# Performance work log

Hardware: AMD Instinct MI355X
Metric: run time of the kernel (lower is better)

## Reference

```python
import jax, jax.numpy as jnp
import numpy as np

# HardSimMask config (baked constants, matching init_kwargs and repo semantics)
K = 0.5                 # minimum-percentage-of-space parameter
D = 256                 # embedding dim
MIN_SIM_BOUND = -np.sqrt(D)   # l2 + relu activation -> (min, max) = (-sqrt(d), 0)
MAX_SIM_BOUND = 0.0
MIN_SIM = (MAX_SIM_BOUND - MIN_SIM_BOUND) * K + MIN_SIM_BOUND  # threshold


def setup_inputs() -> dict:
    key = jax.random.key(0)
    k1, k2 = jax.random.split(key)
    x = jax.random.normal(k1, (8192, D), dtype=jnp.float32)
    x_n = jax.random.normal(k2, (8192, D), dtype=jnp.float32)
    return {"x": x, "x_n": x_n}


def _neg_l2_cdist(x, x_n):
    # -||x_i - x_n_j||_2 via the Gram-matrix identity (matches torch.cdist p=2)
    x2 = jnp.sum(x * x, axis=1, keepdims=True)          # [N, 1]
    y2 = jnp.sum(x_n * x_n, axis=1, keepdims=True).T    # [1, M]
    d2 = x2 + y2 - 2.0 * (x @ x_n.T)                    # [N, M]
    return -jnp.sqrt(jnp.maximum(d2, 0.0))


def reference(x, x_n):
    sim = _neg_l2_cdist(x, x_n)                         # [N, M]
    mask = sim < MIN_SIM
    # agg is None: sim - masked_fill(inf) == -inf where masked, sim elsewhere
    return jnp.where(mask, -jnp.inf, sim)
```

## Files before the change

kernel.cpp:

```cpp
#include <hip/hip_runtime.h>
#include <cstdint>

typedef unsigned short u16;
typedef __attribute__((ext_vector_type(8))) __bf16 bf16x8;
typedef __attribute__((ext_vector_type(4))) float f32x4;

#define NROWS 8192
#define KDIM  256
#define BM 128
#define BN 128
#define BK 64

__device__ __forceinline__ u16 f2bf(float f) {
  uint32_t u = __builtin_bit_cast(uint32_t, f);
  return (u16)((u + 0x7fffu + ((u >> 16) & 1u)) >> 16);
}

__global__ void __launch_bounds__(256) prep_kernel(const float* __restrict__ src,
                                                   u16* __restrict__ dst,
                                                   float* __restrict__ norms) {
  const int row  = blockIdx.x * 4 + (threadIdx.x >> 6);
  const int lane = threadIdx.x & 63;
  const float4 v = *reinterpret_cast<const float4*>(&src[row * KDIM + lane * 4]);
  float s = v.x * v.x + v.y * v.y + v.z * v.z + v.w * v.w;
#pragma unroll
  for (int off = 32; off > 0; off >>= 1) s += __shfl_down(s, off, 64);
  ushort4 b;
  b.x = f2bf(v.x); b.y = f2bf(v.y); b.z = f2bf(v.z); b.w = f2bf(v.w);
  *reinterpret_cast<ushort4*>(&dst[row * KDIM + lane * 4]) = b;
  if (lane == 0) norms[row] = s;
}

__global__ void __launch_bounds__(256) gemm_mask_kernel(const u16* __restrict__ A,
                                                        const u16* __restrict__ B,
                                                        const float* __restrict__ x2,
                                                        const float* __restrict__ y2,
                                                        float* __restrict__ out) {
  __shared__ __align__(16) u16 sA[BM * BK];
  __shared__ __align__(16) u16 sB[BN * BK];
  const int tid  = threadIdx.x;
  const int wave = tid >> 6;
  const int lane = tid & 63;
  const int bx = blockIdx.x & 63;
  const int by = blockIdx.x >> 6;
  const int rowBase = by * BM;
  const int colBase = bx * BN;
  const int wr = wave >> 1;
  const int wc = wave & 1;

  f32x4 acc[4][4] = {};

  for (int k0 = 0; k0 < KDIM; k0 += BK) {
#pragma unroll
    for (int it = 0; it < 4; ++it) {
      const int e = it * 2048 + tid * 8;
      const int r = e >> 6;
      const int c = e & 63;
      const int ldsOff = it * 2048 + wave * 512;
      __builtin_amdgcn_global_load_lds(
          (const __attribute__((address_space(1))) void*)&A[(size_t)(rowBase + r) * KDIM + k0 + c],
          (__attribute__((address_space(3))) void*)&sA[ldsOff], 16, 0, 0);
      __builtin_amdgcn_global_load_lds(
          (const __attribute__((address_space(1))) void*)&B[(size_t)(colBase + r) * KDIM + k0 + c],
          (__attribute__((address_space(3))) void*)&sB[ldsOff], 16, 0, 0);
    }
    __syncthreads();

#pragma unroll
    for (int kk = 0; kk < BK; kk += 32) {
      const int kO = kk + (lane >> 4) * 8;
      bf16x8 af[4], bfr[4];
#pragma unroll
      for (int m = 0; m < 4; ++m)
        af[m] = *reinterpret_cast<const bf16x8*>(&sA[(wr * 64 + m * 16 + (lane & 15)) * BK + kO]);
#pragma unroll
      for (int n = 0; n < 4; ++n)
        bfr[n] = *reinterpret_cast<const bf16x8*>(&sB[(wc * 64 + n * 16 + (lane & 15)) * BK + kO]);
#pragma unroll
      for (int m = 0; m < 4; ++m)
#pragma unroll
        for (int n = 0; n < 4; ++n)
          acc[m][n] = __builtin_amdgcn_mfma_f32_16x16x32_bf16(bfr[n], af[m], acc[m][n], 0, 0, 0);
    }
    __syncthreads();
  }

  const float SENTINEL = -3.0e38f;
  float4 yv[4];
#pragma unroll
  for (int n = 0; n < 4; ++n)
    yv[n] = *reinterpret_cast<const float4*>(&y2[colBase + wc * 64 + n * 16 + (lane >> 4) * 4]);
#pragma unroll
  for (int m = 0; m < 4; ++m) {
    const int row = rowBase + wr * 64 + m * 16 + (lane & 15);
    const float xr = x2[row];
    float* orow = out + (size_t)row * NROWS + colBase + wc * 64 + (lane >> 4) * 4;
#pragma unroll
    for (int n = 0; n < 4; ++n) {
      float4 o;
      {
        float d2 = fmaxf(xr + yv[n].x - 2.0f * acc[m][n][0], 0.0f);
        float s  = -__builtin_sqrtf(d2);
        o.x = (s < -8.0f) ? SENTINEL : s;
      }
      {
        float d2 = fmaxf(xr + yv[n].y - 2.0f * acc[m][n][1], 0.0f);
        float s  = -__builtin_sqrtf(d2);
        o.y = (s < -8.0f) ? SENTINEL : s;
      }
      {
        float d2 = fmaxf(xr + yv[n].z - 2.0f * acc[m][n][2], 0.0f);
        float s  = -__builtin_sqrtf(d2);
        o.z = (s < -8.0f) ? SENTINEL : s;
      }
      {
        float d2 = fmaxf(xr + yv[n].w - 2.0f * acc[m][n][3], 0.0f);
        float s  = -__builtin_sqrtf(d2);
        o.w = (s < -8.0f) ? SENTINEL : s;
      }
      *reinterpret_cast<float4*>(&orow[n * 16]) = o;
    }
  }
}

extern "C" void kernel_launch(void* const* d_in, const int* in_sizes, int n_in,
                              void* d_out, int out_size, void* d_ws, size_t ws_size,
                              hipStream_t stream) {
  const float* x  = (const float*)d_in[0];
  const float* xn = (const float*)d_in[1];
  float* out = (float*)d_out;

  u16* Xb = (u16*)d_ws;
  u16* Yb = Xb + (size_t)NROWS * KDIM;
  float* x2 = (float*)(Yb + (size_t)NROWS * KDIM);
  float* y2 = x2 + NROWS;

  prep_kernel<<<NROWS / 4, 256, 0, stream>>>(x, Xb, x2);
  prep_kernel<<<NROWS / 4, 256, 0, stream>>>(xn, Yb, y2);
  gemm_mask_kernel<<<dim3(64 * 64), dim3(256), 0, stream>>>(Xb, Yb, x2, y2, out);
}
```

Before: 89.68 us.

## Make GEMM blocks persistent over column tiles with register-resident A and full-K B staging

Each block now holds its 128-row A panel in registers for the full K=256 and loops over 8 column tiles, staging a whole 128x256 B tile into LDS with an XOR swizzle to avoid bank conflicts. The grid shrinks from 4096 to 512 blocks and the B load for the next tile is issued right after the MFMA loop, so it overlaps the epilogue stores. The mask test now compares d2 against 64 before taking the sqrt. In exchange there is heavy register pressure (launch_bounds 256,1), 64KB of LDS per block, and only 512 blocks to keep the GPU busy.

```diff
diff --git a/kernel.cpp b/kernel.cpp
--- a/kernel.cpp
+++ b/kernel.cpp
@@ -7,9 +7,8 @@
 
 #define NROWS 8192
 #define KDIM  256
-#define BM 128
-#define BN 128
-#define BK 64
+#define TILE  128
+#define TPB   8
 
 __device__ __forceinline__ u16 f2bf(float f) {
   uint32_t u = __builtin_bit_cast(uint32_t, f);
@@ -31,95 +30,104 @@
   if (lane == 0) norms[row] = s;
 }
 
-__global__ void __launch_bounds__(256) gemm_mask_kernel(const u16* __restrict__ A,
-                                                        const u16* __restrict__ B,
-                                                        const float* __restrict__ x2,
-                                                        const float* __restrict__ y2,
-                                                        float* __restrict__ out) {
-  __shared__ __align__(16) u16 sA[BM * BK];
-  __shared__ __align__(16) u16 sB[BN * BK];
+__device__ __forceinline__ void stageB(u16* sB, const u16* __restrict__ Bbase, int tid) {
+  const int wave = tid >> 6;
+#pragma unroll
+  for (int it = 0; it < 16; ++it) {
+    const int row = it * 8 + (tid >> 5);
+    const int swz = (row & 15) | ((row & 1) << 4);
+    const int srcSlot = (tid & 31) ^ swz;
+    __builtin_amdgcn_global_load_lds(
+        (const __attribute__((address_space(1))) void*)&Bbase[(size_t)row * KDIM + srcSlot * 8],
+        (__attribute__((address_space(3))) void*)&sB[it * 2048 + wave * 512],
+        16, 0, 0);
+  }
+}
+
+__global__ void __launch_bounds__(256, 1) gemm_mask_kernel(const u16* __restrict__ A,
+                                                           const u16* __restrict__ B,
+                                                           const float* __restrict__ x2,
+                                                           const float* __restrict__ y2,
+                                                           float* __restrict__ out) {
+  __shared__ __align__(16) u16 sB[TILE * KDIM];
   const int tid  = threadIdx.x;
   const int wave = tid >> 6;
   const int lane = tid & 63;
-  const int bx = blockIdx.x & 63;
-  const int by = blockIdx.x >> 6;
-  const int rowBase = by * BM;
-  const int colBase = bx * BN;
-  const int wr = wave >> 1;
-  const int wc = wave & 1;
+  const int lo = lane & 15, hi = lane >> 4;
+  const int wr = wave >> 1, wc = wave & 1;
+  const int rowPanel = blockIdx.x >> 3;
+  const int colGroup = blockIdx.x & 7;
+  const int rowBase  = rowPanel * TILE;
 
-  f32x4 acc[4][4] = {};
+  stageB(sB, B + (size_t)(colGroup * TPB) * TILE * KDIM, tid);
 
-  for (int k0 = 0; k0 < KDIM; k0 += BK) {
+  bf16x8 af[4][8];
 #pragma unroll
-    for (int it = 0; it < 4; ++it) {
-      const int e = it * 2048 + tid * 8;
-      const int r = e >> 6;
-      const int c = e & 63;
-      const int ldsOff = it * 2048 + wave * 512;
-      __builtin_amdgcn_global_load_lds(
-          (const __attribute__((address_space(1))) void*)&A[(size_t)(rowBase + r) * KDIM + k0 + c],
-          (__attribute__((address_space(3))) void*)&sA[ldsOff], 16, 0, 0);
-      __builtin_amdgcn_global_load_lds(
-          (const __attribute__((address_space(1))) void*)&B[(size_t)(colBase + r) * KDIM + k0 + c],
-          (__attribute__((address_space(3))) void*)&sB[ldsOff], 16, 0, 0);
-    }
-    __syncthreads();
+  for (int m = 0; m < 4; ++m) {
+    const u16* arow = A + (size_t)(rowBase + wr * 64 + m * 16 + lo) * KDIM;
+#pragma unroll
+    for (int ks = 0; ks < 8; ++ks)
+      af[m][ks] = *reinterpret_cast<const bf16x8*>(&arow[ks * 32 + hi * 8]);
+  }
+  __syncthreads();
 
+  for (int t = 0; t < TPB; ++t) {
+    const int colTile = colGroup * TPB + t;
+    const int colBase = colTile * TILE;
+
+    f32x4 acc[4][4] = {};
 #pragma unroll
-    for (int kk = 0; kk < BK; kk += 32) {
-      const int kO = kk + (lane >> 4) * 8;
-      bf16x8 af[4], bfr[4];
+    for (int ks = 0; ks < 8; ++ks) {
+      bf16x8 bfr[4];
 #pragma unroll
-      for (int m = 0; m < 4; ++m)
-        af[m] = *reinterpret_cast<const bf16x8*>(&sA[(wr * 64 + m * 16 + (lane & 15)) * BK + kO]);
-#pragma unroll
-      for (int n = 0; n < 4; ++n)
-        bfr[n] = *reinterpret_cast<const bf16x8*>(&sB[(wc * 64 + n * 16 + (lane & 15)) * BK + kO]);
+      for (int n = 0; n < 4; ++n) {
+        const int row  = wc * 64 + n * 16 + lo;
+        const int slot = (ks * 4 + hi) ^ ((row & 15) | ((row & 1) << 4));
+        bfr[n] = *reinterpret_cast<const bf16x8*>(&sB[row * KDIM + slot * 8]);
+      }
 #pragma unroll
       for (int m = 0; m < 4; ++m)
 #pragma unroll
         for (int n = 0; n < 4; ++n)
-          acc[m][n] = __builtin_amdgcn_mfma_f32_16x16x32_bf16(bfr[n], af[m], acc[m][n], 0, 0, 0);
+          acc[m][n] = __builtin_amdgcn_mfma_f32_16x16x32_bf16(bfr[n], af[m][ks], acc[m][n], 0, 0, 0);
     }
     __syncthreads();
-  }
+    if (t + 1 < TPB)
+      stageB(sB, B + (size_t)(colTile + 1) * TILE * KDIM, tid);
 
-  const float SENTINEL = -3.0e38f;
-  float4 yv[4];
+    const float SENT = -3.0e38f;
+    float4 yv[4];
 #pragma unroll
-  for (int n = 0; n < 4; ++n)
-    yv[n] = *reinterpret_cast<const float4*>(&y2[colBase + wc * 64 + n * 16 + (lane >> 4) * 4]);
+    for (int n = 0; n < 4; ++n)
+      yv[n] = *reinterpret_cast<const float4*>(&y2[colBase + wc * 64 + n * 16 + hi * 4]);
 #pragma unroll
-  for (int m = 0; m < 4; ++m) {
-    const int row = rowBase + wr * 64 + m * 16 + (lane & 15);
-    const float xr = x2[row];
-    float* orow = out + (size_t)row * NROWS + colBase + wc * 64 + (lane >> 4) * 4;
+    for (int m = 0; m < 4; ++m) {
+      const int row  = rowBase + wr * 64 + m * 16 + lo;
+      const float xr = x2[row];
+      float* orow = out + (size_t)row * NROWS + colBase + wc * 64 + hi * 4;
 #pragma unroll
-    for (int n = 0; n < 4; ++n) {
-      float4 o;
-      {
-        float d2 = fmaxf(xr + yv[n].x - 2.0f * acc[m][n][0], 0.0f);
-        float s  = -__builtin_sqrtf(d2);
-        o.x = (s < -8.0f) ? SENTINEL : s;
+      for (int n = 0; n < 4; ++n) {
+        float4 o;
+        {
+          float d2 = fmaxf(xr + yv[n].x - 2.0f * acc[m][n][0], 0.0f);
+          o.x = (d2 > 64.0f) ? SENT : -__builtin_sqrtf(d2);
+        }
+        {
+          float d2 = fmaxf(xr + yv[n].y - 2.0f * acc[m][n][1], 0.0f);
+          o.y = (d2 > 64.0f) ? SENT : -__builtin_sqrtf(d2);
+        }
+        {
+          float d2 = fmaxf(xr + yv[n].z - 2.0f * acc[m][n][2], 0.0f);
+          o.z = (d2 > 64.0f) ? SENT : -__builtin_sqrtf(d2);
+        }
+        {
+          float d2 = fmaxf(xr + yv[n].w - 2.0f * acc[m][n][3], 0.0f);
+          o.w = (d2 > 64.0f) ? SENT : -__builtin_sqrtf(d2);
+        }
+        *reinterpret_cast<float4*>(&orow[n * 16]) = o;
       }
-      {
-        float d2 = fmaxf(xr + yv[n].y - 2.0f * acc[m][n][1], 0.0f);
-        float s  = -__builtin_sqrtf(d2);
-        o.y = (s < -8.0f) ? SENTINEL : s;
-      }
-      {
-        float d2 = fmaxf(xr + yv[n].z - 2.0f * acc[m][n][2], 0.0f);
-        float s  = -__builtin_sqrtf(d2);
-        o.z = (s < -8.0f) ? SENTINEL : s;
-      }
-      {
-        float d2 = fmaxf(xr + yv[n].w - 2.0f * acc[m][n][3], 0.0f);
-        float s  = -__builtin_sqrtf(d2);
-        o.w = (s < -8.0f) ? SENTINEL : s;
-      }
-      *reinterpret_cast<float4*>(&orow[n * 16]) = o;
     }
+    if (t + 1 < TPB) __syncthreads();
   }
 }
 
@@ -137,5 +145,5 @@
 
   prep_kernel<<<NROWS / 4, 256, 0, stream>>>(x, Xb, x2);
   prep_kernel<<<NROWS / 4, 256, 0, stream>>>(xn, Yb, y2);
-  gemm_mask_kernel<<<dim3(64 * 64), dim3(256), 0, stream>>>(Xb, Yb, x2, y2, out);
+  gemm_mask_kernel<<<dim3(512), dim3(256), 0, stream>>>(Xb, Yb, x2, y2, out);
 }
```

Result: slower. 119.7 us (+33.5%).

## Load MFMA fragments directly from global, remap blocks per XCD, stream output nontemporally

Applied to the files above, without the earlier changes.

Removes the LDS staging and barriers, so each wave loads its bf16 fragments straight from global memory into registers across the full K=256. Block indices are remapped so neighbouring column tiles land on the same XCD for L2 reuse. Output is written with nontemporal stores to avoid polluting cache, and the threshold test uses d2>64 instead of comparing after the sqrt. The risk is redundant global loads with no LDS sharing between waves, and exposed load latency with no pipelining.

```diff
diff --git a/kernel.cpp b/kernel.cpp
--- a/kernel.cpp
+++ b/kernel.cpp
@@ -7,9 +7,6 @@
 
 #define NROWS 8192
 #define KDIM  256
-#define BM 128
-#define BN 128
-#define BK 64
 
 __device__ __forceinline__ u16 f2bf(float f) {
   uint32_t u = __builtin_bit_cast(uint32_t, f);
@@ -36,89 +33,76 @@
                                                         const float* __restrict__ x2,
                                                         const float* __restrict__ y2,
                                                         float* __restrict__ out) {
-  __shared__ __align__(16) u16 sA[BM * BK];
-  __shared__ __align__(16) u16 sB[BN * BK];
   const int tid  = threadIdx.x;
   const int wave = tid >> 6;
   const int lane = tid & 63;
-  const int bx = blockIdx.x & 63;
-  const int by = blockIdx.x >> 6;
-  const int rowBase = by * BM;
-  const int colBase = bx * BN;
-  const int wr = wave >> 1;
-  const int wc = wave & 1;
+  const int lo = lane & 15, hi = lane >> 4;
+  const int wr = wave >> 1, wc = wave & 1;
+
+  const int xcd = blockIdx.x & 7;
+  const int q   = blockIdx.x >> 3;
+  const int bx  = xcd * 8 + (q & 7);
+  const int by  = q >> 3;
+  const int rowBase = by * 128;
+  const int colBase = bx * 128;
+
+  const u16* aRow[4];
+  const u16* bRow[4];
+#pragma unroll
+  for (int m = 0; m < 4; ++m)
+    aRow[m] = A + (size_t)(rowBase + wr * 64 + m * 16 + lo) * KDIM;
+#pragma unroll
+  for (int n = 0; n < 4; ++n)
+    bRow[n] = B + (size_t)(colBase + wc * 64 + n * 16 + lo) * KDIM;
 
   f32x4 acc[4][4] = {};
-
-  for (int k0 = 0; k0 < KDIM; k0 += BK) {
 #pragma unroll
-    for (int it = 0; it < 4; ++it) {
-      const int e = it * 2048 + tid * 8;
-      const int r = e >> 6;
-      const int c = e & 63;
-      const int ldsOff = it * 2048 + wave * 512;
-      __builtin_amdgcn_global_load_lds(
-          (const __attribute__((address_space(1))) void*)&A[(size_t)(rowBase + r) * KDIM + k0 + c],
-          (__attribute__((address_space(3))) void*)&sA[ldsOff], 16, 0, 0);
-      __builtin_amdgcn_global_load_lds(
-          (const __attribute__((address_space(1))) void*)&B[(size_t)(colBase + r) * KDIM + k0 + c],
-          (__attribute__((address_space(3))) void*)&sB[ldsOff], 16, 0, 0);
-    }
-    __syncthreads();
-
+  for (int ks = 0; ks < 8; ++ks) {
+    const int kOff = ks * 32 + hi * 8;
+    bf16x8 af[4], bfr[4];
 #pragma unroll
-    for (int kk = 0; kk < BK; kk += 32) {
-      const int kO = kk + (lane >> 4) * 8;
-      bf16x8 af[4], bfr[4];
+    for (int m = 0; m < 4; ++m)
+      af[m] = *reinterpret_cast<const bf16x8*>(&aRow[m][kOff]);
 #pragma unroll
-      for (int m = 0; m < 4; ++m)
-        af[m] = *reinterpret_cast<const bf16x8*>(&sA[(wr * 64 + m * 16 + (lane & 15)) * BK + kO]);
+    for (int n = 0; n < 4; ++n)
+      bfr[n] = *reinterpret_cast<const bf16x8*>(&bRow[n][kOff]);
+#pragma unroll
+    for (int m = 0; m < 4; ++m)
 #pragma unroll
       for (int n = 0; n < 4; ++n)
-        bfr[n] = *reinterpret_cast<const bf16x8*>(&sB[(wc * 64 + n * 16 + (lane & 15)) * BK + kO]);
-#pragma unroll
-      for (int m = 0; m < 4; ++m)
-#pragma unroll
-        for (int n = 0; n < 4; ++n)
-          acc[m][n] = __builtin_amdgcn_mfma_f32_16x16x32_bf16(bfr[n], af[m], acc[m][n], 0, 0, 0);
-    }
-    __syncthreads();
+        acc[m][n] = __builtin_amdgcn_mfma_f32_16x16x32_bf16(bfr[n], af[m], acc[m][n], 0, 0, 0);
   }
 
-  const float SENTINEL = -3.0e38f;
+  const float SENT = -3.0e38f;
   float4 yv[4];
 #pragma unroll
   for (int n = 0; n < 4; ++n)
-    yv[n] = *reinterpret_cast<const float4*>(&y2[colBase + wc * 64 + n * 16 + (lane >> 4) * 4]);
+    yv[n] = *reinterpret_cast<const float4*>(&y2[colBase + wc * 64 + n * 16 + hi * 4]);
 #pragma unroll
   for (int m = 0; m < 4; ++m) {
-    const int row = rowBase + wr * 64 + m * 16 + (lane & 15);
+    const int row  = rowBase + wr * 64 + m * 16 + lo;
     const float xr = x2[row];
-    float* orow = out + (size_t)row * NROWS + colBase + wc * 64 + (lane >> 4) * 4;
+    float* orow = out + (size_t)row * NROWS + colBase + wc * 64 + hi * 4;
 #pragma unroll
     for (int n = 0; n < 4; ++n) {
-      float4 o;
+      f32x4 o;
       {
         float d2 = fmaxf(xr + yv[n].x - 2.0f * acc[m][n][0], 0.0f);
-        float s  = -__builtin_sqrtf(d2);
-        o.x = (s < -8.0f) ? SENTINEL : s;
+        o[0] = (d2 > 64.0f) ? SENT : -__builtin_sqrtf(d2);
       }
       {
         float d2 = fmaxf(xr + yv[n].y - 2.0f * acc[m][n][1], 0.0f);
-        float s  = -__builtin_sqrtf(d2);
-        o.y = (s < -8.0f) ? SENTINEL : s;
+        o[1] = (d2 > 64.0f) ? SENT : -__builtin_sqrtf(d2);
       }
       {
         float d2 = fmaxf(xr + yv[n].z - 2.0f * acc[m][n][2], 0.0f);
-        float s  = -__builtin_sqrtf(d2);
-        o.z = (s < -8.0f) ? SENTINEL : s;
+        o[2] = (d2 > 64.0f) ? SENT : -__builtin_sqrtf(d2);
       }
       {
         float d2 = fmaxf(xr + yv[n].w - 2.0f * acc[m][n][3], 0.0f);
-        float s  = -__builtin_sqrtf(d2);
-        o.w = (s < -8.0f) ? SENTINEL : s;
+        o[3] = (d2 > 64.0f) ? SENT : -__builtin_sqrtf(d2);
       }
-      *reinterpret_cast<float4*>(&orow[n * 16]) = o;
+      __builtin_nontemporal_store(o, reinterpret_cast<f32x4*>(&orow[n * 16]));
     }
   }
 }
```

New measurement: 174.5 us. 94.6% more time.
